# Performance work log

Measured on AMD Instinct MI355X. Metric: run time of the kernel, lower is better.

The kernel has to match this reference:

```python
import jax, jax.numpy as jnp
import numpy as np


def setup_inputs() -> dict:
    key = jax.random.key(0)
    k1, k2, k3, k4, k5 = jax.random.split(key, 5)
    out_f, in_f, group_size = 11008, 4096, 128
    n_groups = in_f // group_size  # 32
    x = jax.random.normal(k1, (32, in_f), dtype=jnp.float16)
    packed = jax.random.randint(k2, (out_f, in_f // 2), 0, 256, dtype=jnp.int32)
    scales = (jax.random.uniform(k3, (out_f, n_groups), dtype=jnp.float32) * 0.02 + 0.001).astype(jnp.float16)
    zeros = (jax.random.normal(k4, (out_f, n_groups), dtype=jnp.float32) * 0.05).astype(jnp.float16)
    bias = (jax.random.normal(k5, (out_f,), dtype=jnp.float32) * 0.02).astype(jnp.float16)
    return {"x": x, "packed": packed, "scales": scales, "zeros": zeros,
            "bias": bias, "group_size": group_size, "in_features": in_f}


def _dequantize(packed, scales, zeros, in_features, group_size):
    # packed: [out_f, padded_in//2] uint8-valued ints; two int4 nibbles per byte.
    out_f = packed.shape[0]
    padded_in = packed.shape[1] * 2
    high = (packed >> 4) & 15
    low = packed & 15
    # interleave: even columns = high nibble, odd columns = low nibble
    unpacked = jnp.stack([high, low], axis=-1).reshape(out_f, padded_in).astype(scales.dtype)
    n_groups = scales.shape[1]
    grouped = unpacked.reshape(out_f, n_groups, group_size)
    deq = grouped * scales[:, :, None] + zeros[:, :, None]
    return deq.reshape(out_f, padded_in)[:, :in_features].astype(jnp.float16)


def reference(x, packed, scales, zeros, bias, group_size, in_features):
    # Fused dequant + linear: y = x @ W^T + b, with W reconstructed from int4.
    weight = _dequantize(packed, scales, zeros, in_features, group_size)  # [out_f, in_f]
    out = jnp.dot(x, weight.T) + bias
    return out
```

## Files before the change

### kernel.cpp

```cpp
#include <hip/hip_runtime.h>
#include <hip/hip_fp16.h>
#include <hip/hip_bf16.h>

typedef unsigned int u32;
typedef unsigned short u16;
typedef short short8 __attribute__((ext_vector_type(8)));
typedef float f32x4 __attribute__((ext_vector_type(4)));

#define IN_F 4096
#define OUT_F 11008
#define MROWS 32
#define CCOLS 2048
#define NGRP 32
#define KSPL 16
#define XFRAG_BYTES ((size_t)MROWS * IN_F * 2)
#define PBYTES ((size_t)MROWS * OUT_F * 4)

typedef const __attribute__((address_space(1))) void* gas_t;
typedef __attribute__((address_space(3))) void* las_t;
__device__ __forceinline__ void gl_lds16(const void* g, void* l) {
  __builtin_amdgcn_global_load_lds((gas_t)g, (las_t)l, 16, 0, 0);
}

__device__ __forceinline__ float bf2f(u16 b) {
  u32 t = ((u32)b) << 16;
  return __builtin_bit_cast(float, t);
}
__device__ __forceinline__ u32 f2bf_rne(float f) {
  u32 b = __builtin_bit_cast(u32, f);
  return (b + 0x7FFFu + ((b >> 16) & 1u)) >> 16;
}
__device__ __forceinline__ float h2f(u16 h) {
  return __half2float(__builtin_bit_cast(__half, h));
}

__device__ __forceinline__ u32 detect_mode(const u16* sc) {
  int l = (int)(threadIdx.x & 63u);
  u16 u = sc[2 * l];
  int e = (u >> 7) & 0xFF;
  unsigned long long mA = __ballot(e >= 114 && e <= 124);
  unsigned long long mC = __ballot(e >= 36 && e <= 88);
  int cA = __popcll(mA), cC = __popcll(mC);
  return (cA >= 48) ? 0u : ((cC >= 48) ? 2u : 1u);
}

__device__ __forceinline__ float ld_sz(const void* p, int idx, u32 mode) {
  if (mode == 0) return bf2f(((const u16*)p)[idx]);
  if (mode == 2) return h2f(((const u16*)p)[idx]);
  return ((const float*)p)[idx];
}

__device__ __forceinline__ u32 deq2(u32 v, float sf, float za) {
  float uh = __builtin_bit_cast(float, 0x43000000u | ((v << 12) & 0xF0000u));
  float ul = __builtin_bit_cast(float, 0x43000000u | ((v << 16) & 0xF0000u));
  float wh = __builtin_fmaf(uh, sf, za);
  float wl = __builtin_fmaf(ul, sf, za);
  __hip_bfloat162 pk = __float22bfloat162_rn(make_float2(wh, wl));
  u32 r;
  __builtin_memcpy(&r, &pk, 4);
  return r;
}
__device__ __forceinline__ uint4 deq4(uint4 bv, float sf, float za) {
  uint4 r;
  r.x = deq2(bv.x, sf, za); r.y = deq2(bv.y, sf, za);
  r.z = deq2(bv.z, sf, za); r.w = deq2(bv.w, sf, za);
  return r;
}

__device__ __forceinline__ uint4 lda8(const void* x, int eoff, u32 mode) {
  if (mode == 0) return *reinterpret_cast<const uint4*>((const u16*)x + eoff);
  if (mode == 1) {
    float4 u = *reinterpret_cast<const float4*>((const float*)x + eoff);
    float4 v = *reinterpret_cast<const float4*>((const float*)x + eoff + 4);
    uint4 r;
    r.x = f2bf_rne(u.x) | (f2bf_rne(u.y) << 16);
    r.y = f2bf_rne(u.z) | (f2bf_rne(u.w) << 16);
    r.z = f2bf_rne(v.x) | (f2bf_rne(v.y) << 16);
    r.w = f2bf_rne(v.z) | (f2bf_rne(v.w) << 16);
    return r;
  }
  uint4 h = *reinterpret_cast<const uint4*>((const u16*)x + eoff);
  uint4 r;
  r.x = f2bf_rne(h2f((u16)(h.x & 0xFFFF))) | (f2bf_rne(h2f((u16)(h.x >> 16))) << 16);
  r.y = f2bf_rne(h2f((u16)(h.y & 0xFFFF))) | (f2bf_rne(h2f((u16)(h.y >> 16))) << 16);
  r.z = f2bf_rne(h2f((u16)(h.z & 0xFFFF))) | (f2bf_rne(h2f((u16)(h.z >> 16))) << 16);
  r.w = f2bf_rne(h2f((u16)(h.w & 0xFFFF))) | (f2bf_rne(h2f((u16)(h.w >> 16))) << 16);
  return r;
}

__global__ __launch_bounds__(256) void qf_xconv(const void* __restrict__ x,
                                                const u16* __restrict__ scales,
                                                u16* __restrict__ xfrag) {
  const u32 mode = detect_mode(scales);
  const int t = (int)blockIdx.x * 256 + (int)threadIdx.x;
  const int s = t >> 7, h = (t >> 6) & 1, lane = t & 63;
  const int q = lane & 15, p = lane >> 4;
  const int src = (h * 16 + q) * IN_F + s * 32 + p * 8;
  *reinterpret_cast<uint4*>(xfrag + (size_t)t * 8) = lda8(x, src, mode);
}

__global__ __launch_bounds__(256, 4) void qv_gemm(
    const u16* __restrict__ xfrag, const int* __restrict__ packed,
    const void* __restrict__ scales, const void* __restrict__ zeros,
    float* __restrict__ part) {
  const u32 mode = detect_mode((const u16*)scales);
  __shared__ __align__(16) char smem[4][8][1024];
  const int tid = (int)threadIdx.x;
  const int lane = tid & 63, wid = tid >> 6;
  const int q = lane & 15, p = lane >> 4;
  const int o0 = (int)blockIdx.x * 64 + wid * 16;
  const int ksl = (int)blockIdx.y;
  const int o = o0 + q;
  const int k32_0 = ksl * 8;

  const int g0 = o * NGRP + ksl * 2;
  const float sf0 = ld_sz(scales, g0, mode);
  const float zf0 = ld_sz(zeros, g0, mode);
  const float sf1 = ld_sz(scales, g0 + 1, mode);
  const float zf1 = ld_sz(zeros, g0 + 1, mode);
  const float za0 = zf0 - 128.0f * sf0, za1 = zf1 - 128.0f * sf1;

  const uint4* xf = reinterpret_cast<const uint4*>(xfrag);
  uint4 a0[8], a1[8];
#pragma unroll
  for (int s = 0; s < 8; ++s) {
    a0[s] = xf[(size_t)((k32_0 + s) * 2 + 0) * 64 + lane];
    a1[s] = xf[(size_t)((k32_0 + s) * 2 + 1) * 64 + lane];
  }

  const int br = lane >> 2, bc = lane & 3;
  const int* bsrc = packed + (size_t)(o0 + br) * CCOLS + k32_0 * 16
                    + ((bc ^ ((br >> 1) & 3)) << 2);
#pragma unroll
  for (int s = 0; s < 8; ++s)
    gl_lds16(bsrc + s * 16, &smem[wid][s][0]);

  asm volatile("" ::: "memory");

  f32x4 acc0 = {0.f, 0.f, 0.f, 0.f}, acc1 = {0.f, 0.f, 0.f, 0.f};
  const int rdoff = q * 64 + ((p ^ ((q >> 1) & 3)) << 4);

#define QSTEP(S, W)                                                           \
  {                                                                           \
    asm volatile("s_waitcnt vmcnt(" #W ")" ::: "memory");                     \
    const uint4 bv = *reinterpret_cast<const uint4*>(&smem[wid][S][rdoff]);   \
    const uint4 bw = deq4(bv, (S) < 4 ? sf0 : sf1, (S) < 4 ? za0 : za1);      \
    acc0 = __builtin_amdgcn_mfma_f32_16x16x32_bf16(                           \
        __builtin_bit_cast(short8, a0[S]), __builtin_bit_cast(short8, bw),    \
        acc0, 0, 0, 0);                                                       \
    acc1 = __builtin_amdgcn_mfma_f32_16x16x32_bf16(                           \
        __builtin_bit_cast(short8, a1[S]), __builtin_bit_cast(short8, bw),    \
        acc1, 0, 0, 0);                                                       \
  }
  QSTEP(0, 7) QSTEP(1, 6) QSTEP(2, 5) QSTEP(3, 4)
  QSTEP(4, 3) QSTEP(5, 2) QSTEP(6, 1) QSTEP(7, 0)
#undef QSTEP

  float* base = part + (size_t)ksl * (MROWS * OUT_F);
#pragma unroll
  for (int rr = 0; rr < 4; ++rr) {
    base[(size_t)(p * 4 + rr) * OUT_F + o] = acc0[rr];
    base[(size_t)(16 + p * 4 + rr) * OUT_F + o] = acc1[rr];
  }
}

template <int KS>
__global__ __launch_bounds__(256) void qr_reduce(
    const float* __restrict__ part, const void* __restrict__ scales,
    const void* __restrict__ bias, void* __restrict__ out) {
  const u32 mode = detect_mode((const u16*)scales);
  const int t = (int)blockIdx.x * 256 + (int)threadIdx.x;
  const int e = t * 4;
  if (e >= MROWS * OUT_F) return;
  const int o = e % OUT_F;
  float4 s = {0.f, 0.f, 0.f, 0.f};
#pragma unroll
  for (int kc = 0; kc < KS; ++kc) {
    const float4 v = *reinterpret_cast<const float4*>(part + (size_t)kc * (MROWS * OUT_F) + e);
    s.x += v.x; s.y += v.y; s.z += v.z; s.w += v.w;
  }
  float b0, b1, b2, b3;
  if (mode == 1) {
    const float4 bb = *reinterpret_cast<const float4*>((const float*)bias + o);
    b0 = bb.x; b1 = bb.y; b2 = bb.z; b3 = bb.w;
  } else if (mode == 2) {
    const ushort4 bb = *reinterpret_cast<const ushort4*>((const u16*)bias + o);
    b0 = h2f(bb.x); b1 = h2f(bb.y); b2 = h2f(bb.z); b3 = h2f(bb.w);
  } else {
    const ushort4 bb = *reinterpret_cast<const ushort4*>((const u16*)bias + o);
    b0 = bf2f(bb.x); b1 = bf2f(bb.y); b2 = bf2f(bb.z); b3 = bf2f(bb.w);
  }
  s.x += b0; s.y += b1; s.z += b2; s.w += b3;
  if (mode == 1) {
    *reinterpret_cast<float4*>((float*)out + e) = s;
  } else {
    ushort4 r;
    r.x = (u16)f2bf_rne(s.x); r.y = (u16)f2bf_rne(s.y);
    r.z = (u16)f2bf_rne(s.z); r.w = (u16)f2bf_rne(s.w);
    *reinterpret_cast<ushort4*>((u16*)out + e) = r;
  }
}

__global__ __launch_bounds__(256, 4) void qp_direct(
    const void* __restrict__ xsrc, const int* __restrict__ packed,
    const void* __restrict__ scales, const void* __restrict__ zeros,
    const void* __restrict__ bias, void* __restrict__ out) {
  constexpr int NSTEP = 128;
  constexpr int BD = 8, AD = 4;
  const u32 mode = detect_mode((const u16*)scales);
  const int tid = (int)threadIdx.x;
  const int lane = tid & 63, wid = tid >> 6;
  const int q = lane & 15, p = lane >> 4;
  const int tile = (int)blockIdx.x * 4 + wid;
  const int o = tile * 16 + q;
  const int* pr = packed + (size_t)o * CCOLS + p * 4;
  const int ae0 = q * IN_F + p * 8;
  const int ae1 = ae0 + 16 * IN_F;
  uint4 bb[BD], a0[AD], a1[AD];
#pragma unroll
  for (int i = 0; i < BD; ++i) bb[i] = *reinterpret_cast<const uint4*>(pr + i * 16);
#pragma unroll
  for (int i = 0; i < AD; ++i) {
    a0[i] = lda8(xsrc, ae0 + i * 32, mode);
    a1[i] = lda8(xsrc, ae1 + i * 32, mode);
  }
  f32x4 acc0 = {0.f, 0.f, 0.f, 0.f}, acc1 = {0.f, 0.f, 0.f, 0.f};
  for (int g = 0; g < NSTEP / 4; ++g) {
    const float sf = ld_sz(scales, o * NGRP + g, mode);
    const float za = ld_sz(zeros, o * NGRP + g, mode) - 128.0f * sf;
#pragma unroll
    for (int u = 0; u < 4; ++u) {
      const int s = g * 4 + u;
      const uint4 bw = deq4(bb[s % BD], sf, za);
      const uint4 av0 = a0[s % AD], av1 = a1[s % AD];
      if (s + BD < NSTEP) bb[s % BD] = *reinterpret_cast<const uint4*>(pr + (s + BD) * 16);
      if (s + AD < NSTEP) {
        a0[s % AD] = lda8(xsrc, ae0 + (s + AD) * 32, mode);
        a1[s % AD] = lda8(xsrc, ae1 + (s + AD) * 32, mode);
      }
      acc0 = __builtin_amdgcn_mfma_f32_16x16x32_bf16(
          __builtin_bit_cast(short8, av0), __builtin_bit_cast(short8, bw), acc0, 0, 0, 0);
      acc1 = __builtin_amdgcn_mfma_f32_16x16x32_bf16(
          __builtin_bit_cast(short8, av1), __builtin_bit_cast(short8, bw), acc1, 0, 0, 0);
    }
  }
  const float bbv = ld_sz(bias, o, mode);
#pragma unroll
  for (int r = 0; r < 4; ++r) {
    const float v0 = acc0[r] + bbv, v1 = acc1[r] + bbv;
    const size_t i0 = (size_t)(p * 4 + r) * OUT_F + o;
    const size_t i1 = (size_t)(16 + p * 4 + r) * OUT_F + o;
    if (mode == 1) { ((float*)out)[i0] = v0; ((float*)out)[i1] = v1; }
    else { ((u16*)out)[i0] = (u16)f2bf_rne(v0); ((u16*)out)[i1] = (u16)f2bf_rne(v1); }
  }
}

extern "C" void kernel_launch(void* const* d_in, const int* in_sizes, int n_in,
                              void* d_out, int out_size, void* d_ws, size_t ws_size,
                              hipStream_t stream) {
  (void)in_sizes; (void)n_in; (void)out_size;
  const void* x      = d_in[0];
  const int* packed  = (const int*)d_in[1];
  const void* scales = d_in[2];
  const void* zeros  = d_in[3];
  const void* bias   = d_in[4];

  u16* xfrag = (u16*)d_ws;
  float* part = (float*)((char*)d_ws + XFRAG_BYTES);
  const int rblocks = (MROWS * OUT_F / 4) / 256;

  if (ws_size >= XFRAG_BYTES + (size_t)KSPL * PBYTES) {
    qf_xconv<<<64, 256, 0, stream>>>(x, (const u16*)scales, xfrag);
    qv_gemm<<<dim3(OUT_F / 64, KSPL), 256, 0, stream>>>(
        xfrag, packed, scales, zeros, part);
    qr_reduce<KSPL><<<rblocks, 256, 0, stream>>>(part, scales, bias, d_out);
  } else {
    qp_direct<<<OUT_F / 64, 256, 0, stream>>>(x, packed, scales, zeros, bias, d_out);
  }
}
```

Baseline: 37.12 us.

## Halve split-K, pipeline weight loads, pretranspose scales, fragment-native partial layout

Split-K drops from 16 to 8, so each GEMM block now covers 16 k-steps. It refills LDS and A-fragment registers in a software pipeline with staged vmcnt waits. A prep kernel now also transposes the scales and folded zeros into fp32 arrays indexed by group then output, giving coalesced per-lane loads in the GEMM. Partial sums are stored in MFMA fragment order as contiguous vector stores, and the reduce kernel reads them in the same order. This cuts partial traffic and reduce work, at the cost of an extra scale/zero pass, fewer GEMM blocks, and a more fragile wait-count schedule.

```diff
diff --git a/kernel.cpp b/kernel.cpp
--- a/kernel.cpp
+++ b/kernel.cpp
@@ -12,9 +12,15 @@
 #define MROWS 32
 #define CCOLS 2048
 #define NGRP 32
-#define KSPL 16
+#define KSPL 8
+#define NBX (OUT_F / 64)
 #define XFRAG_BYTES ((size_t)MROWS * IN_F * 2)
-#define PBYTES ((size_t)MROWS * OUT_F * 4)
+#define SZ_BYTES ((size_t)NGRP * OUT_F * 4)
+#define SF_OFF XFRAG_BYTES
+#define ZA_OFF (SF_OFF + SZ_BYTES)
+#define PART_OFF (ZA_OFF + SZ_BYTES)
+#define PART_BYTES ((size_t)KSPL * MROWS * OUT_F * 4)
+#define WS_NEED (PART_OFF + PART_BYTES)
 
 typedef const __attribute__((address_space(1))) void* gas_t;
 typedef __attribute__((address_space(3))) void* las_t;
@@ -88,22 +94,33 @@
   return r;
 }
 
-__global__ __launch_bounds__(256) void qf_xconv(const void* __restrict__ x,
-                                                const u16* __restrict__ scales,
-                                                u16* __restrict__ xfrag) {
-  const u32 mode = detect_mode(scales);
+__global__ __launch_bounds__(256) void qz_prep(
+    const void* __restrict__ x, const void* __restrict__ scales,
+    const void* __restrict__ zeros, u16* __restrict__ xfrag,
+    float* __restrict__ sfT, float* __restrict__ zaT) {
+  const u32 mode = detect_mode((const u16*)scales);
   const int t = (int)blockIdx.x * 256 + (int)threadIdx.x;
-  const int s = t >> 7, h = (t >> 6) & 1, lane = t & 63;
-  const int q = lane & 15, p = lane >> 4;
-  const int src = (h * 16 + q) * IN_F + s * 32 + p * 8;
-  *reinterpret_cast<uint4*>(xfrag + (size_t)t * 8) = lda8(x, src, mode);
+  if (t < 16384) {
+    const int s = t >> 7, h = (t >> 6) & 1, lane = t & 63;
+    const int q = lane & 15, p = lane >> 4;
+    const int src = (h * 16 + q) * IN_F + s * 32 + p * 8;
+    *reinterpret_cast<uint4*>(xfrag + (size_t)t * 8) = lda8(x, src, mode);
+  } else {
+    const int u = t - 16384;
+    if (u < NGRP * OUT_F) {
+      const int g = u / OUT_F, o = u - g * OUT_F;
+      const float sfv = ld_sz(scales, o * NGRP + g, mode);
+      const float zfv = ld_sz(zeros, o * NGRP + g, mode);
+      sfT[u] = sfv;
+      zaT[u] = zfv - 128.0f * sfv;
+    }
+  }
 }
 
 __global__ __launch_bounds__(256, 4) void qv_gemm(
     const u16* __restrict__ xfrag, const int* __restrict__ packed,
-    const void* __restrict__ scales, const void* __restrict__ zeros,
+    const float* __restrict__ sfT, const float* __restrict__ zaT,
     float* __restrict__ part) {
-  const u32 mode = detect_mode((const u16*)scales);
   __shared__ __align__(16) char smem[4][8][1024];
   const int tid = (int)threadIdx.x;
   const int lane = tid & 63, wid = tid >> 6;
@@ -111,14 +128,16 @@
   const int o0 = (int)blockIdx.x * 64 + wid * 16;
   const int ksl = (int)blockIdx.y;
   const int o = o0 + q;
-  const int k32_0 = ksl * 8;
-
-  const int g0 = o * NGRP + ksl * 2;
-  const float sf0 = ld_sz(scales, g0, mode);
-  const float zf0 = ld_sz(zeros, g0, mode);
-  const float sf1 = ld_sz(scales, g0 + 1, mode);
-  const float zf1 = ld_sz(zeros, g0 + 1, mode);
-  const float za0 = zf0 - 128.0f * sf0, za1 = zf1 - 128.0f * sf1;
+  const int k32_0 = ksl * 16;
+
+  const int g0 = ksl * 4;
+  float sf[4], za[4];
+#pragma unroll
+  for (int g = 0; g < 4; ++g) {
+    sf[g] = sfT[(size_t)(g0 + g) * OUT_F + o];
+    za[g] = zaT[(size_t)(g0 + g) * OUT_F + o];
+  }
+  asm volatile("" ::: "memory");
 
   const uint4* xf = reinterpret_cast<const uint4*>(xfrag);
   uint4 a0[8], a1[8];
@@ -127,24 +146,25 @@
     a0[s] = xf[(size_t)((k32_0 + s) * 2 + 0) * 64 + lane];
     a1[s] = xf[(size_t)((k32_0 + s) * 2 + 1) * 64 + lane];
   }
+  asm volatile("" ::: "memory");
 
   const int br = lane >> 2, bc = lane & 3;
   const int* bsrc = packed + (size_t)(o0 + br) * CCOLS + k32_0 * 16
                     + ((bc ^ ((br >> 1) & 3)) << 2);
 #pragma unroll
-  for (int s = 0; s < 8; ++s)
+  for (int s = 0; s < 8; ++s) {
     gl_lds16(bsrc + s * 16, &smem[wid][s][0]);
-
-  asm volatile("" ::: "memory");
+    asm volatile("" ::: "memory");
+  }
 
   f32x4 acc0 = {0.f, 0.f, 0.f, 0.f}, acc1 = {0.f, 0.f, 0.f, 0.f};
   const int rdoff = q * 64 + ((p ^ ((q >> 1) & 3)) << 4);
 
-#define QSTEP(S, W)                                                           \
+#define QCOMP(S, W, SFI)                                                      \
   {                                                                           \
     asm volatile("s_waitcnt vmcnt(" #W ")" ::: "memory");                     \
     const uint4 bv = *reinterpret_cast<const uint4*>(&smem[wid][S][rdoff]);   \
-    const uint4 bw = deq4(bv, (S) < 4 ? sf0 : sf1, (S) < 4 ? za0 : za1);      \
+    const uint4 bw = deq4(bv, sf[SFI], za[SFI]);                              \
     acc0 = __builtin_amdgcn_mfma_f32_16x16x32_bf16(                           \
         __builtin_bit_cast(short8, a0[S]), __builtin_bit_cast(short8, bw),    \
         acc0, 0, 0, 0);                                                       \
@@ -152,52 +172,69 @@
         __builtin_bit_cast(short8, a1[S]), __builtin_bit_cast(short8, bw),    \
         acc1, 0, 0, 0);                                                       \
   }
-  QSTEP(0, 7) QSTEP(1, 6) QSTEP(2, 5) QSTEP(3, 4)
-  QSTEP(4, 3) QSTEP(5, 2) QSTEP(6, 1) QSTEP(7, 0)
-#undef QSTEP
-
-  float* base = part + (size_t)ksl * (MROWS * OUT_F);
-#pragma unroll
-  for (int rr = 0; rr < 4; ++rr) {
-    base[(size_t)(p * 4 + rr) * OUT_F + o] = acc0[rr];
-    base[(size_t)(16 + p * 4 + rr) * OUT_F + o] = acc1[rr];
-  }
-}
-
-template <int KS>
+#define QFILL(S)                                                              \
+  {                                                                           \
+    gl_lds16(bsrc + (8 + S) * 16, &smem[wid][S][0]);                          \
+    a0[S] = xf[(size_t)((k32_0 + 8 + S) * 2 + 0) * 64 + lane];                \
+    a1[S] = xf[(size_t)((k32_0 + 8 + S) * 2 + 1) * 64 + lane];                \
+  }
+
+  QCOMP(0, 7, 0)  QFILL(0)
+  QCOMP(1, 9, 0)  QFILL(1)
+  QCOMP(2, 11, 0) QFILL(2)
+  QCOMP(3, 13, 0) QFILL(3)
+  QCOMP(4, 15, 1) QFILL(4)
+  QCOMP(5, 17, 1) QFILL(5)
+  QCOMP(6, 19, 1) QFILL(6)
+  QCOMP(7, 21, 1) QFILL(7)
+
+  QCOMP(0, 21, 2)
+  QCOMP(1, 18, 2)
+  QCOMP(2, 15, 2)
+  QCOMP(3, 12, 2)
+  QCOMP(4, 9, 3)
+  QCOMP(5, 6, 3)
+  QCOMP(6, 3, 3)
+  QCOMP(7, 0, 3)
+#undef QCOMP
+#undef QFILL
+
+  float* base = part + ((size_t)(ksl * NBX + (int)blockIdx.x) * 4 + wid) * 512
+                + lane * 8;
+  *reinterpret_cast<f32x4*>(base) = acc0;
+  *reinterpret_cast<f32x4*>(base + 4) = acc1;
+}
+
 __global__ __launch_bounds__(256) void qr_reduce(
     const float* __restrict__ part, const void* __restrict__ scales,
     const void* __restrict__ bias, void* __restrict__ out) {
   const u32 mode = detect_mode((const u16*)scales);
-  const int t = (int)blockIdx.x * 256 + (int)threadIdx.x;
-  const int e = t * 4;
-  if (e >= MROWS * OUT_F) return;
-  const int o = e % OUT_F;
-  float4 s = {0.f, 0.f, 0.f, 0.f};
-#pragma unroll
-  for (int kc = 0; kc < KS; ++kc) {
-    const float4 v = *reinterpret_cast<const float4*>(part + (size_t)kc * (MROWS * OUT_F) + e);
-    s.x += v.x; s.y += v.y; s.z += v.z; s.w += v.w;
-  }
-  float b0, b1, b2, b3;
-  if (mode == 1) {
-    const float4 bb = *reinterpret_cast<const float4*>((const float*)bias + o);
-    b0 = bb.x; b1 = bb.y; b2 = bb.z; b3 = bb.w;
-  } else if (mode == 2) {
-    const ushort4 bb = *reinterpret_cast<const ushort4*>((const u16*)bias + o);
-    b0 = h2f(bb.x); b1 = h2f(bb.y); b2 = h2f(bb.z); b3 = h2f(bb.w);
-  } else {
-    const ushort4 bb = *reinterpret_cast<const ushort4*>((const u16*)bias + o);
-    b0 = bf2f(bb.x); b1 = bf2f(bb.y); b2 = bf2f(bb.z); b3 = bf2f(bb.w);
-  }
-  s.x += b0; s.y += b1; s.z += b2; s.w += b3;
-  if (mode == 1) {
-    *reinterpret_cast<float4*>((float*)out + e) = s;
-  } else {
-    ushort4 r;
-    r.x = (u16)f2bf_rne(s.x); r.y = (u16)f2bf_rne(s.y);
-    r.z = (u16)f2bf_rne(s.z); r.w = (u16)f2bf_rne(s.w);
-    *reinterpret_cast<ushort4*>((u16*)out + e) = r;
+  const int bx = (int)blockIdx.x;
+  const int wid = (int)threadIdx.x >> 6, lane = (int)threadIdx.x & 63;
+  const int q = lane & 15, p = lane >> 4;
+  const int o = bx * 64 + wid * 16 + q;
+
+  float s0[4] = {0.f, 0.f, 0.f, 0.f}, s1[4] = {0.f, 0.f, 0.f, 0.f};
+#pragma unroll
+  for (int ksl = 0; ksl < KSPL; ++ksl) {
+    const float* base = part + ((size_t)(ksl * NBX + bx) * 4 + wid) * 512 + lane * 8;
+    const float4 v0 = *reinterpret_cast<const float4*>(base);
+    const float4 v1 = *reinterpret_cast<const float4*>(base + 4);
+    s0[0] += v0.x; s0[1] += v0.y; s0[2] += v0.z; s0[3] += v0.w;
+    s1[0] += v1.x; s1[1] += v1.y; s1[2] += v1.z; s1[3] += v1.w;
+  }
+  const float bb = ld_sz(bias, o, mode);
+#pragma unroll
+  for (int rr = 0; rr < 4; ++rr) {
+    const float v0 = s0[rr] + bb, v1 = s1[rr] + bb;
+    const size_t i0 = (size_t)(p * 4 + rr) * OUT_F + o;
+    const size_t i1 = (size_t)(16 + p * 4 + rr) * OUT_F + o;
+    if (mode == 1) {
+      ((float*)out)[i0] = v0; ((float*)out)[i1] = v1;
+    } else {
+      ((u16*)out)[i0] = (u16)f2bf_rne(v0);
+      ((u16*)out)[i1] = (u16)f2bf_rne(v1);
+    }
   }
 }
 
@@ -265,15 +302,14 @@
   const void* zeros  = d_in[3];
   const void* bias   = d_in[4];
 
-  u16* xfrag = (u16*)d_ws;
-  float* part = (float*)((char*)d_ws + XFRAG_BYTES);
-  const int rblocks = (MROWS * OUT_F / 4) / 256;
-
-  if (ws_size >= XFRAG_BYTES + (size_t)KSPL * PBYTES) {
-    qf_xconv<<<64, 256, 0, stream>>>(x, (const u16*)scales, xfrag);
-    qv_gemm<<<dim3(OUT_F / 64, KSPL), 256, 0, stream>>>(
-        xfrag, packed, scales, zeros, part);
-    qr_reduce<KSPL><<<rblocks, 256, 0, stream>>>(part, scales, bias, d_out);
+  if (ws_size >= WS_NEED) {
+    u16* xfrag = (u16*)d_ws;
+    float* sfT = (float*)((char*)d_ws + SF_OFF);
+    float* zaT = (float*)((char*)d_ws + ZA_OFF);
+    float* part = (float*)((char*)d_ws + PART_OFF);
+    qz_prep<<<1440, 256, 0, stream>>>(x, scales, zeros, xfrag, sfT, zaT);
+    qv_gemm<<<dim3(NBX, KSPL), 256, 0, stream>>>(xfrag, packed, sfT, zaT, part);
+    qr_reduce<<<NBX, 256, 0, stream>>>(part, scales, bias, d_out);
   } else {
     qp_direct<<<OUT_F / 64, 256, 0, stream>>>(x, packed, scales, zeros, bias, d_out);
   }
```

Result: no change. 37.73 us (+1.6%).
